# Optimization experiments

Hardware: AMD Instinct MI355X
Metric: run time of the kernel (lower is better)

## Reference

```python
import jax, jax.numpy as jnp
import numpy as np

D_MODEL = 2048
NUM_HEADS = 16
THETA = 10000.0


def setup_inputs() -> dict:
    key = jax.random.key(0)
    ks = jax.random.split(key, 5)
    bs, S, d = 4, 2048, D_MODEL
    std = (2.0 / (d + d)) ** 0.5
    x = jax.random.normal(ks[0], (bs, S, d), dtype=jnp.float32)
    wq = jax.random.normal(ks[1], (d, d), dtype=jnp.float32) * std
    wk = jax.random.normal(ks[2], (d, d), dtype=jnp.float32) * std
    wv = jax.random.normal(ks[3], (d, d), dtype=jnp.float32) * std
    wo = jax.random.normal(ks[4], (d, d), dtype=jnp.float32) * std
    return {"x": x, "wq": wq, "wk": wk, "wv": wv, "wo": wo}


def _rope(t, cos, sin):
    # t: (bs, H, S, d_k); cos/sin: (S, d_k) interleaved-duplicated
    # rotate_half: (-x1, x0, -x3, x2, ...)
    x_even = t[..., 0::2]
    x_odd = t[..., 1::2]
    rot = jnp.stack((-x_odd, x_even), axis=-1).reshape(t.shape)
    return t * cos + rot * sin


def reference(x, wq, wk, wv, wo):
    bs, S, d = x.shape
    H = NUM_HEADS
    dk = d // H
    # QKV projections (Linear has no bias; weight stored (out, in), applied as x @ W.T)
    q = (x @ wq.T).reshape(bs, S, H, dk).transpose(0, 2, 1, 3)  # (bs,H,S,dk)
    k = (x @ wk.T).reshape(bs, S, H, dk).transpose(0, 2, 1, 3)
    v = (x @ wv.T).reshape(bs, S, H, dk).transpose(0, 2, 1, 3)

    # RoPE tables (interleaved convention)
    half = dk // 2
    inv_freq = THETA ** (-2.0 * jnp.arange(half, dtype=jnp.float32) / dk)  # (half,)
    pos = jnp.arange(S, dtype=jnp.float32)
    ang = pos[:, None] * inv_freq[None, :]  # (S, half)
    cos = jnp.repeat(jnp.cos(ang), 2, axis=-1)  # (S, dk), (c0,c0,c1,c1,...)
    sin = jnp.repeat(jnp.sin(ang), 2, axis=-1)
    q = _rope(q, cos, sin)
    k = _rope(k, cos, sin)

    scale = 1.0 / jnp.sqrt(jnp.asarray(dk, dtype=x.dtype))
    attn = jnp.einsum("bhqd,bhkd->bhqk", q, k) * scale  # (bs,H,S,S)
    causal = jnp.tril(jnp.ones((S, S), dtype=bool))
    attn = jnp.where(causal, attn, -jnp.inf)
    probs = jax.nn.softmax(attn, axis=-1)
    out = jnp.einsum("bhqk,bhkd->bhqd", probs, v)  # (bs,H,S,dk)
    out = out.transpose(0, 2, 1, 3).reshape(bs, S, d)
    return out @ wo.T
```

## Files before the change

kernel.cpp:

```cpp
#include <hip/hip_runtime.h>
#include <hip/hip_bf16.h>
#include <cstdint>
#include <cstddef>

typedef unsigned short u16;
typedef unsigned int u32;
typedef __attribute__((ext_vector_type(8))) short short8;
typedef __attribute__((ext_vector_type(4))) short bfx4;
typedef __attribute__((ext_vector_type(4))) float f32x4;

#define D_MODEL 2048
#define SEQ     2048
#define BATCH   4
#define NHEADS  16
#define DKH     128
#define NTOK    (BATCH*SEQ)

typedef const __attribute__((address_space(1))) void* gptr_t;
typedef __attribute__((address_space(3))) void* lptr_t;

__device__ inline float bf2f(u16 u) {
  union { float f; u32 i; } x; x.i = ((u32)u) << 16; return x.f;
}
__device__ inline u16 f2bf(float f) {
  union { float f; u32 i; } x; x.f = f;
  return (u16)((x.i + 0x7FFFu + ((x.i >> 16) & 1u)) >> 16);
}
__device__ inline u32 packbf2(float a, float b) {
  union { float f; u32 i; } xa, xb; xa.f = a; xb.f = b;
  return (xa.i >> 16) | (xb.i & 0xFFFF0000u);
}

__global__ void cvt_kernel(const float* __restrict__ in, u16* __restrict__ out, int n8) {
  int i = blockIdx.x * 256 + threadIdx.x;
  if (i >= n8) return;
  const float* p = in + (size_t)i * 8;
  short8 v;
#pragma unroll
  for (int j = 0; j < 8; ++j) v[j] = (short)f2bf(p[j]);
  *(short8*)(out + (size_t)i * 8) = v;
}

__global__ void cvtw_kernel(const float* __restrict__ wq, const float* __restrict__ wk,
                            const float* __restrict__ wv, const float* __restrict__ wo,
                            u16* __restrict__ wall) {
  int by = blockIdx.y;
  const float* src = by == 0 ? wq : by == 1 ? wk : by == 2 ? wv : wo;
  int i = blockIdx.x * 256 + threadIdx.x;
  const float* p = src + (size_t)i * 8;
  short8 v;
#pragma unroll
  for (int j = 0; j < 8; ++j) v[j] = (short)f2bf(p[j]);
  *(short8*)(wall + (size_t)by * D_MODEL * D_MODEL + (size_t)i * 8) = v;
}

__global__ void trig_kernel(float* __restrict__ cosT, float* __restrict__ sinT) {
  int i = blockIdx.x * 256 + threadIdx.x;
  int s = i >> 6, j = i & 63;
  float inv = powf(10000.0f, -2.0f * (float)j / 128.0f);
  float ang = (float)s * inv;
  cosT[i] = cosf(ang);
  sinT[i] = sinf(ang);
}

template<int MODE>
__global__ __launch_bounds__(512, 2)
void gemm_bt256(const u16* __restrict__ A, const u16* __restrict__ B,
                void* __restrict__ Cv, int M, int N, int K) {
  __shared__ u16 lds[2][2][256 * 64];
  const int T = threadIdx.x;
  const int lane = T & 63, w = T >> 6;
  const int lo = lane & 15, hi = lane >> 4;
  const int wr = w >> 2, wc = w & 3;
  int bm, bn;
  if (MODE == 2) {
    int sid = (blockIdx.x & 7) * 96 + (blockIdx.x >> 3);
    bm = (sid / 24) * 256; bn = (sid % 24) * 256;
  } else {
    bm = (blockIdx.x >> 3) * 256; bn = (blockIdx.x & 7) * 256;
  }
  const int nt = K >> 6;

  const int qrow_base = (w & 3) * 8 + (w >> 2) * 128;
  const int lrow = lane >> 3;
  const int lchunk = lane & 7;

  auto STAGEQ = [&](int buf, int z, int kt) {
    int r0 = z * 32 + qrow_base;
    int rn = r0 + lrow;
    int ck = lchunk ^ (rn & 7);
    __builtin_amdgcn_global_load_lds(
        (gptr_t)(A + (size_t)(bm + rn) * K + kt * 64 + ck * 8),
        (lptr_t)(&lds[buf][0][0] + r0 * 64), 16, 0, 0);
    __builtin_amdgcn_global_load_lds(
        (gptr_t)(B + (size_t)(bn + rn) * K + kt * 64 + ck * 8),
        (lptr_t)(&lds[buf][1][0] + r0 * 64), 16, 0, 0);
  };

  f32x4 acc[8][4] = {};
  short8 bfrag[4][2];

#define GPHASE(qq, tt, cc) do {                                                \
    short8 af[2][2];                                                           \
    _Pragma("unroll")                                                          \
    for (int m2 = 0; m2 < 2; ++m2) {                                           \
      int row = wr * 128 + (2 * (qq) + m2) * 16 + lo;                          \
      _Pragma("unroll")                                                        \
      for (int c = 0; c < 2; ++c)                                              \
        af[m2][c] = *(const short8*)((const char*)&lds[cc][0][0] +             \
            (row << 7) + ((c * 64 + hi * 16) ^ ((row & 7) << 4)));             \
    }                                                                          \
    if ((qq) == 0) {                                                           \
      _Pragma("unroll")                                                        \
      for (int ni = 0; ni < 4; ++ni) {                                         \
        int row = wc * 64 + ni * 16 + lo;                                      \
        _Pragma("unroll")                                                      \
        for (int c = 0; c < 2; ++c)                                            \
          bfrag[ni][c] = *(const short8*)((const char*)&lds[cc][1][0] +        \
              (row << 7) + ((c * 64 + hi * 16) ^ ((row & 7) << 4)));           \
      }                                                                        \
    }                                                                          \
    { int zz = ((qq) + 3) & 3;                                                 \
      int stt = (qq) == 0 ? (tt) + 1 : (tt) + 2;                               \
      int sbuf = (qq) == 0 ? ((tt) + 1) & 1 : (tt) & 1;                        \
      if (stt < nt) STAGEQ(sbuf, zz, stt); }                                   \
    __builtin_amdgcn_s_barrier();                                              \
    asm volatile("s_waitcnt lgkmcnt(0)" ::: "memory");                         \
    __builtin_amdgcn_sched_barrier(0);                                         \
    __builtin_amdgcn_s_setprio(1);                                             \
    _Pragma("unroll")                                                          \
    for (int m2 = 0; m2 < 2; ++m2)                                             \
      _Pragma("unroll")                                                        \
      for (int ni = 0; ni < 4; ++ni)                                           \
        _Pragma("unroll")                                                      \
        for (int c = 0; c < 2; ++c)                                            \
          acc[2 * (qq) + m2][ni] = __builtin_amdgcn_mfma_f32_16x16x32_bf16(    \
              af[m2][c], bfrag[ni][c], acc[2 * (qq) + m2][ni], 0, 0, 0);       \
    __builtin_amdgcn_s_setprio(0);                                             \
    __builtin_amdgcn_sched_barrier(0);                                         \
    __builtin_amdgcn_s_barrier();                                              \
  } while (0)

#pragma unroll
  for (int z = 0; z < 4; ++z) STAGEQ(0, z, 0);
#pragma unroll
  for (int z = 0; z < 3; ++z) STAGEQ(1, z, 1);
  asm volatile("s_waitcnt vmcnt(6)" ::: "memory");
  __builtin_amdgcn_s_barrier();

  for (int t = 0; t < nt; ++t) {
    const int cur = t & 1;
    GPHASE(0, t, cur);
    GPHASE(1, t, cur);
    GPHASE(2, t, cur);
    GPHASE(3, t, cur);
    if (t == nt - 2) asm volatile("s_waitcnt vmcnt(0)" ::: "memory");
    else             asm volatile("s_waitcnt vmcnt(6)" ::: "memory");
    __builtin_amdgcn_s_barrier();
  }
#undef GPHASE

#pragma unroll
  for (int mi = 0; mi < 8; ++mi)
#pragma unroll
    for (int ni = 0; ni < 4; ++ni) {
      int row = bm + wr * 128 + mi * 16 + hi * 4;
      int col = bn + wc * 64 + ni * 16 + lo;
#pragma unroll
      for (int r = 0; r < 4; ++r) {
        if (MODE == 1) {
          ((float*)Cv)[(size_t)(row + r) * N + col] = acc[mi][ni][r];
        } else if (MODE == 2) {
          int buf = col >> 11, colw = col & 2047;
          ((u16*)Cv)[(size_t)buf * NTOK * D_MODEL +
                     (size_t)(row + r) * D_MODEL + colw] = f2bf(acc[mi][ni][r]);
        } else {
          ((u16*)Cv)[(size_t)(row + r) * N + col] = f2bf(acc[mi][ni][r]);
        }
      }
    }
}

__global__ void rope_kernel(u16* __restrict__ t, const float* __restrict__ cosT,
                            const float* __restrict__ sinT, float premul) {
  int i = blockIdx.x * 256 + threadIdx.x;
  int row = i >> 8;
  int g = i & 255;
  int s = row & (SEQ - 1);
  int col = g << 3;
  int j0 = (col & 127) >> 1;
  short8 v = *(short8*)(t + (size_t)row * D_MODEL + col);
#pragma unroll
  for (int p = 0; p < 4; ++p) {
    float c  = cosT[s * 64 + j0 + p];
    float sn = sinT[s * 64 + j0 + p];
    float e = bf2f((u16)v[2 * p]), o = bf2f((u16)v[2 * p + 1]);
    v[2 * p]     = (short)f2bf((e * c - o * sn) * premul);
    v[2 * p + 1] = (short)f2bf((o * c + e * sn) * premul);
  }
  *(short8*)(t + (size_t)row * D_MODEL + col) = v;
}

__global__ void vt_kernel(const u16* __restrict__ V, u16* __restrict__ VT) {
  __shared__ u16 tbuf[64][66];
  int bh = blockIdx.z;
  int b = bh >> 4, h = bh & 15;
  int s0 = blockIdx.x << 6, d0 = blockIdx.y << 6;
  for (int i = threadIdx.x; i < 512; i += 256) {
    int sr = i >> 3, c8 = (i & 7) << 3;
    short8 v = *(const short8*)(V + (size_t)(b * SEQ + s0 + sr) * D_MODEL + h * DKH + d0 + c8);
#pragma unroll
    for (int j = 0; j < 8; ++j) tbuf[sr][c8 + j] = (u16)v[j];
  }
  __syncthreads();
  for (int i = threadIdx.x; i < 512; i += 256) {
    int dr = i >> 3, s8 = (i & 7) << 3;
    short8 v;
#pragma unroll
    for (int j = 0; j < 8; ++j) v[j] = (short)tbuf[s8 + j][dr];
    *(short8*)(VT + ((size_t)bh * DKH + d0 + dr) * SEQ + s0 + s8) = v;
  }
}

__device__ __forceinline__ void attn_qtile(
    int qt, int b, int h, int bh,
    const u16* __restrict__ Q, const u16* __restrict__ K,
    const u16* __restrict__ VT, u16* __restrict__ O,
    const float* __restrict__ cosT, const float* __restrict__ sinT,
    u16 (*Ksb)[64 * 128], u16 (*Vsb)[128 * 64], u16* Pw)
{
  const int T = threadIdx.x, lane = T & 63, w = T >> 6;
  const int lo = lane & 15, hi = lane >> 4;
  const int q0 = qt << 6;
  const int qrow = q0 + w * 16 + lo;
  const int swzC = (lo & 7) << 4;
  const float SC = 0.08838834764831845f * 1.4426950408889634f;

  const u16* Qp = Q + (size_t)(b * SEQ + qrow) * D_MODEL + h * DKH;
  const float* cp = cosT + qrow * 64;
  const float* sp = sinT + qrow * 64;
  short8 qf[4];
#pragma unroll
  for (int c = 0; c < 4; ++c) {
    short8 v = *(const short8*)(Qp + c * 32 + hi * 8);
#pragma unroll
    for (int p = 0; p < 4; ++p) {
      float cc = cp[c * 16 + hi * 4 + p] * SC;
      float sn = sp[c * 16 + hi * 4 + p] * SC;
      float e = bf2f((u16)v[2 * p]), o = bf2f((u16)v[2 * p + 1]);
      v[2 * p]     = (short)f2bf(e * cc - o * sn);
      v[2 * p + 1] = (short)f2bf(o * cc + e * sn);
    }
    qf[c] = v;
  }

  f32x4 ot[8] = {};
  float m = -1e30f, l = 0.f;

  const u16* Kbase = K + ((size_t)b * SEQ) * D_MODEL + h * DKH;
  const u16* Vbase = VT + (size_t)bh * DKH * SEQ;

  auto STAGE = [&](int buf, int kt2) {
    const int kb2 = kt2 << 6;
#pragma unroll
    for (int q = 0; q < 4; ++q) {
      int base = q * 256 + (T & 192);
      int s = base + lane;
      int kv = s >> 4, ck = (s & 15) ^ (kv & 7);
      __builtin_amdgcn_global_load_lds(
          (gptr_t)(Kbase + (size_t)(kb2 + kv) * D_MODEL + ck * 8),
          (lptr_t)(Ksb[buf] + (size_t)base * 8), 16, 0, 0);
      int d = s >> 3, cv2 = (s & 7) ^ (d & 7);
      __builtin_amdgcn_global_load_lds(
          (gptr_t)(Vbase + (size_t)d * SEQ + kb2 + cv2 * 8),
          (lptr_t)(Vsb[buf] + (size_t)base * 8), 16, 0, 0);
    }
  };

  STAGE(0, 0);
  __syncthreads();
  int cur = 0;

  for (int kt = 0; kt <= qt; ++kt) {
    if (kt < qt) STAGE(cur ^ 1, kt + 1);
    const int kb = kt << 6;
    const u16* Ks = Ksb[cur];
    const u16* Vs = Vsb[cur];

    f32x4 sa[4];
    __builtin_amdgcn_s_setprio(1);
#pragma unroll
    for (int g = 0; g < 4; ++g) {
      f32x4 s4 = {0.f, 0.f, 0.f, 0.f};
      int krow = g * 16 + lo;
#pragma unroll
      for (int c = 0; c < 4; ++c) {
        int o = ((krow << 8) + c * 64 + hi * 16) ^ ((krow & 7) << 4);
        short8 kf = *(const short8*)((const char*)Ks + o);
        s4 = __builtin_amdgcn_mfma_f32_16x16x32_bf16(kf, qf[c], s4, 0, 0, 0);
      }
      sa[g] = s4;
    }
    __builtin_amdgcn_s_setprio(0);

    const bool diag = (kt == qt);
    float pm = -1e30f;
#pragma unroll
    for (int g = 0; g < 4; ++g)
#pragma unroll
      for (int r = 0; r < 4; ++r) {
        float sv = sa[g][r];
        if (diag && (kb + g * 16 + hi * 4 + r) > qrow) sv = -1e30f;
        sa[g][r] = sv;
        pm = fmaxf(pm, sv);
      }
    pm = fmaxf(pm, __shfl_xor(pm, 16));
    pm = fmaxf(pm, __shfl_xor(pm, 32));

    if (!__all(pm <= m + 8.0f)) {
      float mn = fmaxf(m, pm);
      float sc = __builtin_amdgcn_exp2f(m - mn);
      l *= sc;
#pragma unroll
      for (int g2 = 0; g2 < 8; ++g2)
#pragma unroll
        for (int r = 0; r < 4; ++r) ot[g2][r] *= sc;
      m = mn;
    }

    float rs = 0.f;
#pragma unroll
    for (int g = 0; g < 4; ++g) {
      float p0 = __builtin_amdgcn_exp2f(sa[g][0] - m);
      float p1 = __builtin_amdgcn_exp2f(sa[g][1] - m);
      float p2 = __builtin_amdgcn_exp2f(sa[g][2] - m);
      float p3 = __builtin_amdgcn_exp2f(sa[g][3] - m);
      rs += (p0 + p1) + (p2 + p3);
      int off = lo * 128 + ((g * 32 + hi * 8) ^ swzC);
      *(u32*)((char*)Pw + off)     = packbf2(p0, p1);
      *(u32*)((char*)Pw + off + 4) = packbf2(p2, p3);
    }
    rs += __shfl_xor(rs, 16);
    rs += __shfl_xor(rs, 32);
    l += rs;

    __builtin_amdgcn_s_setprio(1);
#pragma unroll
    for (int c2 = 0; c2 < 2; ++c2) {
      short8 pf = *(const short8*)((char*)Pw + lo * 128 + ((c2 * 64 + hi * 16) ^ swzC));
#pragma unroll
      for (int g2 = 0; g2 < 8; ++g2) {
        int vrow = g2 * 16 + lo;
        int vo = ((vrow << 7) + c2 * 64 + hi * 16) ^ ((vrow & 7) << 4);
        short8 vf = *(const short8*)((const char*)Vs + vo);
        ot[g2] = __builtin_amdgcn_mfma_f32_16x16x32_bf16(vf, pf, ot[g2], 0, 0, 0);
      }
    }
    __builtin_amdgcn_s_setprio(0);

    __syncthreads();
    cur ^= 1;
  }

  float invl = 1.0f / l;
  u16* Op = O + (size_t)(b * SEQ + qrow) * D_MODEL + h * DKH + hi * 4;
#pragma unroll
  for (int g2 = 0; g2 < 8; ++g2) {
    bfx4 v4;
#pragma unroll
    for (int r = 0; r < 4; ++r) v4[r] = (short)f2bf(ot[g2][r] * invl);
    *(bfx4*)(Op + g2 * 16) = v4;
  }
}

__global__ __launch_bounds__(256)
void attn_kernel(const u16* __restrict__ Q, const u16* __restrict__ K,
                 const u16* __restrict__ VT, u16* __restrict__ O,
                 const float* __restrict__ cosT, const float* __restrict__ sinT) {
  __shared__ u16 Ksb[2][64 * 128];
  __shared__ u16 Vsb[2][128 * 64];
  __shared__ u16 Ps[4 * 16 * 64];
  const int wg = blockIdx.x;
  const int xcd = wg & 7, idx = wg >> 3;
  const int bh = xcd * 8 + (idx >> 4);
  const int pair = idx & 15;
  const int b = bh >> 4, h = bh & 15;
  u16* Pw = Ps + (threadIdx.x >> 6) * 1024;
#pragma unroll 1
  for (int side = 0; side < 2; ++side) {
    const int qt = side ? pair : 31 - pair;
    attn_qtile(qt, b, h, bh, Q, K, VT, O, cosT, sinT, Ksb, Vsb, Pw);
  }
}

extern "C" void kernel_launch(void* const* d_in, const int* in_sizes, int n_in,
                              void* d_out, int out_size, void* d_ws, size_t ws_size,
                              hipStream_t stream) {
  const float* x  = (const float*)d_in[0];
  const float* wq = (const float*)d_in[1];
  const float* wk = (const float*)d_in[2];
  const float* wv = (const float*)d_in[3];
  const float* wo = (const float*)d_in[4];
  float* out = (float*)d_out;

  const size_t TOKB = (size_t)NTOK * D_MODEL * 2;
  const size_t WB   = (size_t)D_MODEL * D_MODEL * 2;
  char* p = (char*)d_ws;
  u16* xb  = (u16*)p; p += TOKB;
  u16* wqb = (u16*)p; p += WB;
  u16* wkb = (u16*)p; p += WB;
  u16* wvb = (u16*)p; p += WB;
  u16* wob = (u16*)p; p += WB;
  u16* Qb  = (u16*)p; p += TOKB;
  u16* Kb  = (u16*)p; p += TOKB;
  u16* Vb  = (u16*)p; p += TOKB;
  u16* VTb = (u16*)p; p += TOKB;
  u16* Ob  = (u16*)p; p += TOKB;
  float* cosT = (float*)p; p += (size_t)SEQ * 64 * 4;
  float* sinT = (float*)p; p += (size_t)SEQ * 64 * 4;
  (void)wkb; (void)wvb;

  cvt_kernel<<<8192, 256, 0, stream>>>(x, xb, 2097152);
  cvtw_kernel<<<dim3(2048, 4), 256, 0, stream>>>(wq, wk, wv, wo, wqb);
  trig_kernel<<<512, 256, 0, stream>>>(cosT, sinT);

  gemm_bt256<2><<<768, 512, 0, stream>>>(xb, wqb, Qb, NTOK, 6144, D_MODEL);

  rope_kernel<<<8192, 256, 0, stream>>>(Kb, cosT, sinT, 1.0f);

  vt_kernel<<<dim3(32, 2, 64), 256, 0, stream>>>(Vb, VTb);

  attn_kernel<<<1024, 256, 0, stream>>>(Qb, Kb, VTb, Ob, cosT, sinT);

  gemm_bt256<1><<<256, 512, 0, stream>>>(Ob, wob, out, NTOK, D_MODEL, D_MODEL);
}
```

Baseline: 469.0 us.

## Fuse K RoPE and V transpose into the QKV GEMM epilogue

The QKV projection GEMM epilogue now applies RoPE to the K section, using a lane shuffle to fetch the even/odd partner. It also writes V directly in transposed per-head layout, so the separate rope_kernel and vt_kernel launches and the V round trip through memory go away. The cost is a heavier epilogue with cos/sin gathers and strided 4-element VT stores, which may coalesce less well than the old LDS-based transpose. K is now rounded to bf16 once after RoPE rather than before and after.

New measurement: 460.8 us. No clear change (-1.7%).

```diff
diff --git a/kernel.cpp b/kernel.cpp
--- a/kernel.cpp
+++ b/kernel.cpp
@@ -66,7 +66,8 @@
 template<int MODE>
 __global__ __launch_bounds__(512, 2)
 void gemm_bt256(const u16* __restrict__ A, const u16* __restrict__ B,
-                void* __restrict__ Cv, int M, int N, int K) {
+                void* __restrict__ Cv, int M, int N, int K,
+                const float* __restrict__ cosT, const float* __restrict__ sinT) {
   __shared__ u16 lds[2][2][256 * 64];
   const int T = threadIdx.x;
   const int lane = T & 63, w = T >> 6;
@@ -160,65 +161,59 @@
   }
 #undef GPHASE
 
-#pragma unroll
-  for (int mi = 0; mi < 8; ++mi)
-#pragma unroll
-    for (int ni = 0; ni < 4; ++ni) {
-      int row = bm + wr * 128 + mi * 16 + hi * 4;
-      int col = bn + wc * 64 + ni * 16 + lo;
-#pragma unroll
-      for (int r = 0; r < 4; ++r) {
-        if (MODE == 1) {
-          ((float*)Cv)[(size_t)(row + r) * N + col] = acc[mi][ni][r];
-        } else if (MODE == 2) {
-          int buf = col >> 11, colw = col & 2047;
-          ((u16*)Cv)[(size_t)buf * NTOK * D_MODEL +
-                     (size_t)(row + r) * D_MODEL + colw] = f2bf(acc[mi][ni][r]);
+  if (MODE == 2) {
+    u16* Qb = (u16*)Cv;
+    u16* Kb = Qb + (size_t)NTOK * D_MODEL;
+    u16* VT = Qb + 2 * (size_t)NTOK * D_MODEL;
+    const int buf = bn >> 11;
+#pragma unroll
+    for (int mi = 0; mi < 8; ++mi)
+#pragma unroll
+      for (int ni = 0; ni < 4; ++ni) {
+        int row = bm + wr * 128 + mi * 16 + hi * 4;
+        int colw = (bn & 2047) + wc * 64 + ni * 16 + lo;
+        if (buf == 0) {
+#pragma unroll
+          for (int r = 0; r < 4; ++r)
+            Qb[(size_t)(row + r) * D_MODEL + colw] = f2bf(acc[mi][ni][r]);
+        } else if (buf == 1) {
+          int j0 = (colw & 127) >> 1;
+          int odd = colw & 1;
+#pragma unroll
+          for (int r = 0; r < 4; ++r) {
+            float v = acc[mi][ni][r];
+            float pv = __shfl_xor(v, 1);
+            int s = (row + r) & (SEQ - 1);
+            float c  = cosT[s * 64 + j0];
+            float sn = sinT[s * 64 + j0];
+            float outv = odd ? (v * c + pv * sn) : (v * c - pv * sn);
+            Kb[(size_t)(row + r) * D_MODEL + colw] = f2bf(outv);
+          }
         } else {
-          ((u16*)Cv)[(size_t)(row + r) * N + col] = f2bf(acc[mi][ni][r]);
+          int bh = ((row >> 11) << 4) + (colw >> 7);
+          int d = colw & 127;
+          int s = row & (SEQ - 1);
+          bfx4 v4;
+#pragma unroll
+          for (int r = 0; r < 4; ++r) v4[r] = (short)f2bf(acc[mi][ni][r]);
+          *(bfx4*)(VT + ((size_t)bh * DKH + d) * SEQ + s) = v4;
         }
       }
-    }
-}
-
-__global__ void rope_kernel(u16* __restrict__ t, const float* __restrict__ cosT,
-                            const float* __restrict__ sinT, float premul) {
-  int i = blockIdx.x * 256 + threadIdx.x;
-  int row = i >> 8;
-  int g = i & 255;
-  int s = row & (SEQ - 1);
-  int col = g << 3;
-  int j0 = (col & 127) >> 1;
-  short8 v = *(short8*)(t + (size_t)row * D_MODEL + col);
-#pragma unroll
-  for (int p = 0; p < 4; ++p) {
-    float c  = cosT[s * 64 + j0 + p];
-    float sn = sinT[s * 64 + j0 + p];
-    float e = bf2f((u16)v[2 * p]), o = bf2f((u16)v[2 * p + 1]);
-    v[2 * p]     = (short)f2bf((e * c - o * sn) * premul);
-    v[2 * p + 1] = (short)f2bf((o * c + e * sn) * premul);
-  }
-  *(short8*)(t + (size_t)row * D_MODEL + col) = v;
-}
-
-__global__ void vt_kernel(const u16* __restrict__ V, u16* __restrict__ VT) {
-  __shared__ u16 tbuf[64][66];
-  int bh = blockIdx.z;
-  int b = bh >> 4, h = bh & 15;
-  int s0 = blockIdx.x << 6, d0 = blockIdx.y << 6;
-  for (int i = threadIdx.x; i < 512; i += 256) {
-    int sr = i >> 3, c8 = (i & 7) << 3;
-    short8 v = *(const short8*)(V + (size_t)(b * SEQ + s0 + sr) * D_MODEL + h * DKH + d0 + c8);
-#pragma unroll
-    for (int j = 0; j < 8; ++j) tbuf[sr][c8 + j] = (u16)v[j];
-  }
-  __syncthreads();
-  for (int i = threadIdx.x; i < 512; i += 256) {
-    int dr = i >> 3, s8 = (i & 7) << 3;
-    short8 v;
-#pragma unroll
-    for (int j = 0; j < 8; ++j) v[j] = (short)tbuf[s8 + j][dr];
-    *(short8*)(VT + ((size_t)bh * DKH + d0 + dr) * SEQ + s0 + s8) = v;
+  } else {
+#pragma unroll
+    for (int mi = 0; mi < 8; ++mi)
+#pragma unroll
+      for (int ni = 0; ni < 4; ++ni) {
+        int row = bm + wr * 128 + mi * 16 + hi * 4;
+        int col = bn + wc * 64 + ni * 16 + lo;
+#pragma unroll
+        for (int r = 0; r < 4; ++r) {
+          if (MODE == 1)
+            ((float*)Cv)[(size_t)(row + r) * N + col] = acc[mi][ni][r];
+          else
+            ((u16*)Cv)[(size_t)(row + r) * N + col] = f2bf(acc[mi][ni][r]);
+        }
+      }
   }
 }
 
@@ -407,30 +402,24 @@
   const size_t WB   = (size_t)D_MODEL * D_MODEL * 2;
   char* p = (char*)d_ws;
   u16* xb  = (u16*)p; p += TOKB;
-  u16* wqb = (u16*)p; p += WB;
-  u16* wkb = (u16*)p; p += WB;
-  u16* wvb = (u16*)p; p += WB;
-  u16* wob = (u16*)p; p += WB;
+  u16* wqb = (u16*)p; p += 4 * WB;
+  u16* wob = wqb + 3 * (size_t)D_MODEL * D_MODEL;
   u16* Qb  = (u16*)p; p += TOKB;
   u16* Kb  = (u16*)p; p += TOKB;
-  u16* Vb  = (u16*)p; p += TOKB;
   u16* VTb = (u16*)p; p += TOKB;
   u16* Ob  = (u16*)p; p += TOKB;
   float* cosT = (float*)p; p += (size_t)SEQ * 64 * 4;
   float* sinT = (float*)p; p += (size_t)SEQ * 64 * 4;
-  (void)wkb; (void)wvb;
 
   cvt_kernel<<<8192, 256, 0, stream>>>(x, xb, 2097152);
   cvtw_kernel<<<dim3(2048, 4), 256, 0, stream>>>(wq, wk, wv, wo, wqb);
   trig_kernel<<<512, 256, 0, stream>>>(cosT, sinT);
 
-  gemm_bt256<2><<<768, 512, 0, stream>>>(xb, wqb, Qb, NTOK, 6144, D_MODEL);
-
-  rope_kernel<<<8192, 256, 0, stream>>>(Kb, cosT, sinT, 1.0f);
-
-  vt_kernel<<<dim3(32, 2, 64), 256, 0, stream>>>(Vb, VTb);
+  gemm_bt256<2><<<768, 512, 0, stream>>>(xb, wqb, Qb, NTOK, 6144, D_MODEL,
+                                         cosT, sinT);
 
   attn_kernel<<<1024, 256, 0, stream>>>(Qb, Kb, VTb, Ob, cosT, sinT);
 
-  gemm_bt256<1><<<256, 512, 0, stream>>>(Ob, wob, out, NTOK, D_MODEL, D_MODEL);
-}
+  gemm_bt256<1><<<256, 512, 0, stream>>>(Ob, wob, out, NTOK, D_MODEL, D_MODEL,
+                                         nullptr, nullptr);
+}
```
